# Optimization experiments

Hardware: AMD Instinct MI355X
Metric: run time of the kernel (lower is better)

## Reference

```python
import jax, jax.numpy as jnp
import numpy as np

H = 128   # hidden_size
NL = 3    # num_layers
R = 32    # water_rows (Water2sea_slice_num)
O = 48    # water_cols (Original_slice_len)
B = 64    # batch_size
F = 32    # input_size
L = R + O - 1  # Water2sea_slice_len (wavefront length)


def setup_inputs():
    key = jax.random.key(0)
    k1, k2, k3, k4 = jax.random.split(key, 4)
    stdv = 1.0 / np.sqrt(H)
    inp = jax.random.normal(k1, (B, R, O, F), dtype=jnp.float32)
    W_first = jax.random.uniform(k2, (6 * H, F + 2 * H), minval=-stdv, maxval=stdv, dtype=jnp.float32)
    W_other = jax.random.uniform(k3, (NL - 1, 6 * H, 4 * H), minval=-stdv, maxval=stdv, dtype=jnp.float32)
    Bias = jax.random.uniform(k4, (NL, 6 * H), minval=-stdv, maxval=stdv, dtype=jnp.float32)
    return {"input": inp, "W_first": W_first, "W_other": W_other, "Bias": Bias,
            "batch_size": B, "input_size": F, "flag": 0}


def _forward(inp, W_first, W_other, Bias, batch_size, input_size, flag):
    # permute: flag==0 -> [rows, batch, cols, feat]
    x = jnp.transpose(inp, (2, 0, 1, 3)) if flag == 1 else jnp.transpose(inp, (1, 0, 2, 3))
    Rn, bs, On, Fn = x.shape
    Ln = Rn + On - 1
    # wavefront-shifted input: row r occupies slices [r, r+On) (input_transfer)
    padded = jnp.pad(x, ((0, 0), (0, 0), (0, Rn - 1), (0, 0)))                 # [R,B,L,F]
    shifted = jax.vmap(lambda t, r: jnp.roll(t, r, axis=1))(padded, jnp.arange(Rn))
    a0 = shifted.reshape(Rn * bs, Ln, Fn)
    # bias applied to row-group g at slice s iff (s < Rn) and (g <= s)  [faithful to linear()]
    s_idx = jnp.arange(Ln)[:, None]
    g_idx = jnp.arange(Rn)[None, :]
    bias_mask = ((g_idx <= s_idx) & (s_idx < Rn)).astype(jnp.float32)          # [L,R]
    bias_mask = jnp.repeat(bias_mask, bs, axis=1)[..., None]                   # [L,RB,1]

    def run_layer(a, W, bvec):
        # a: [RB, L, feat]; W: [6H, feat+2H]; bvec: [6H]
        def step(carry, xs):
            h_row, h_col = carry
            a_s, m_s = xs
            z = jnp.concatenate([h_row, h_col, a_s], axis=-1)
            gate = z @ W.T + m_s * bvec                                        # [RB,6H]
            sig = jax.nn.sigmoid(gate[:, :4 * H])
            tnh = jnp.tanh(gate[:, 4 * H:])
            ur, orow, uc, ocol = jnp.split(sig, 4, axis=-1)
            ir, ic = jnp.split(tnh, 2, axis=-1)
            h_row_n = jnp.tanh((1.0 - ur) * h_row + ur * ir) * orow
            h_col_n = jnp.tanh((1.0 - uc) * h_col + uc * ic) * ocol
            out = jnp.concatenate([h_row_n, h_col_n], axis=-1)
            h_col_roll = jnp.roll(h_col_n, bs, axis=0)  # transfer col hidden to next row
            return (h_row_n, h_col_roll), (out, h_row_n, h_col_n)
        h0 = jnp.zeros((Rn * bs, H), a.dtype)
        _, (outs, hrows, hcols) = jax.lax.scan(step, (h0, h0), (jnp.swapaxes(a, 0, 1), bias_mask))
        return outs, hrows, hcols  # each [L, RB, *]

    row_saves, col_saves = [], []
    a = a0
    for layer in range(NL):
        W = W_first if layer == 0 else W_other[layer - 1]
        outs, hrows, hcols = run_layer(a, W, Bias[layer])
        hrows = hrows.reshape(Ln, Rn, bs, H)
        hcols = hcols.reshape(Ln, Rn, bs, H)
        # row r finishes at slice On-1+r; col hidden of last row-group saved for slices >= Rn-1
        row_saves.append(hrows[On - 1 + jnp.arange(Rn), jnp.arange(Rn)])       # [R,B,H]
        col_saves.append(hcols[Rn - 1:, Rn - 1])                               # [O,B,H]
        a = jnp.swapaxes(outs, 0, 1)                                           # [RB,L,2H]; dropout p=0 -> identity
    output_all_slice = a
    hidden_row_all = jnp.transpose(jnp.stack(row_saves), (2, 0, 1, 3))         # [B,NL,R,H]
    hidden_col_all = jnp.transpose(jnp.stack(col_saves), (2, 0, 1, 3))         # [B,NL,O,H]
    return output_all_slice, hidden_row_all, hidden_col_all


def reference(input, W_first, W_other, Bias, batch_size, input_size, flag):
    return _forward(input, W_first, W_other, Bias, batch_size, input_size, flag)
```

## Files before the change

### kernel.cpp

```cpp
#include <hip/hip_runtime.h>
#include <stdint.h>

#define HH   128
#define NLAY 3
#define RR   32
#define OO   48
#define BBX  64
#define FFX  32
#define LLX  (RR + OO - 1)
#define RBr  (RR * BBX)
#define N6   (6 * HH)
#define TSTEPS (LLX + NLAY - 1)
#define NBLOCKS 192

typedef unsigned short u16;
typedef __attribute__((ext_vector_type(8))) short short8;
typedef __attribute__((ext_vector_type(4))) float f32x4;

#define OFF_ABUF0 ((size_t)0)
#define SZ_ABUF0  ((size_t)LLX * RBr * FFX * 2)
#define OFF_HZ    (OFF_ABUF0 + SZ_ABUF0)
#define SZ_HZ     ((size_t)NLAY * 2 * RBr * 256 * 2)
#define OFF_BAR   (OFF_HZ + SZ_HZ)
#define SZ_BAR    ((size_t)4096)
#define SZ_STATE  (SZ_HZ + SZ_BAR)

__device__ __forceinline__ u16 f2b(float x) {
  uint32_t u = __float_as_uint(x);
  return (u16)((u + 0x7FFFu + ((u >> 16) & 1u)) >> 16);
}
__device__ __forceinline__ float rcp_(float x) { return __builtin_amdgcn_rcpf(x); }
__device__ __forceinline__ float sigmoidf_(float x) {
  return rcp_(1.0f + __expf(-x));
}
__device__ __forceinline__ float tanhf_(float x) {
  return 1.0f - 2.0f * rcp_(__expf(2.0f * x) + 1.0f);
}

__global__ __launch_bounds__(256) void k_prep_input(const float* __restrict__ inp,
                                                    u16* __restrict__ abuf0) {
  int idx = blockIdx.x * 256 + threadIdx.x;
  if (idx >= LLX * RBr * FFX) return;
  int f   = idx & (FFX - 1);
  int row = (idx >> 5) & (RBr - 1);
  int s   = idx / (RBr * FFX);
  int g = row >> 6, b = row & 63;
  int o = s - g;
  float v = (o >= 0 && o < OO) ? inp[((b * RR + g) * OO + o) * FFX + f] : 0.0f;
  abuf0[idx] = f2b(v);
}

__global__ __launch_bounds__(256) void k_zero(uint32_t* __restrict__ p, size_t nwords) {
  size_t i = (size_t)blockIdx.x * 256 + threadIdx.x;
  size_t stride = (size_t)gridDim.x * 256;
  for (; i < nwords; i += stride) p[i] = 0u;
}

__device__ __forceinline__ void step_barrier(uint32_t* barC, uint32_t target, bool light) {
  __syncthreads();
  if (threadIdx.x == 0) {
    if (!light) __threadfence();
    __hip_atomic_fetch_add(barC, 1u, __ATOMIC_RELAXED, __HIP_MEMORY_SCOPE_AGENT);
    while (__hip_atomic_load(barC, __ATOMIC_RELAXED, __HIP_MEMORY_SCOPE_AGENT) < target)
      __builtin_amdgcn_s_sleep(1);
    if (!light) __threadfence();
  }
  __syncthreads();
  if (light) asm volatile("buffer_inv" ::: "memory");
}

template <int KK>
__device__ __forceinline__ void stage_w(const float* __restrict__ Wsrc, int jblk,
                                        u16* __restrict__ Wl) {
  constexpr int NFRAG = (KK / 32) * 6;
  for (int e = threadIdx.x; e < NFRAG * 64; e += 512) {
    int kcm = e >> 6, ln = e & 63;
    int kc = kcm / 6, m = kcm - kc * 6;
    int fr2 = ln & 15, hi2 = ln >> 4;
    int srow = m * 128 + jblk * 16 + fr2;
    const float* src = Wsrc + (size_t)srow * KK + kc * 32 + hi2 * 8;
    short8 v;
#pragma unroll
    for (int x = 0; x < 8; ++x) v[x] = (short)f2b(src[x]);
    *(short8*)&Wl[(size_t)e * 8] = v;
  }
}

template <int KK>
__device__ __forceinline__ void persist_body(char* __restrict__ ws,
                                             const float* __restrict__ Bias_l,
                                             float* __restrict__ out,
                                             int layer, int jblk, int bblk, bool light,
                                             u16* __restrict__ Wl,
                                             float* __restrict__ hcl,
                                             uint32_t* __restrict__ barC) {
  constexpr int NCH = KK / 32;
  const int tid = threadIdx.x;
  const int lane = tid & 63, w = tid >> 6;
  const int fr = lane & 15, hi = lane >> 4;

  const int g0   = w * 4 + (fr >> 3);
  const int bcol = bblk * 8 + (fr & 7);
  const int arow[2] = { g0 * 64 + bcol, (g0 + 2) * 64 + bcol };
  const int arp[2]  = { ((g0 + 1) & 31) * 64 + bcol, ((g0 + 3) & 31) * 64 + bcol };
  const int j = jblk * 16 + fr;
  const u16* wfrag = &Wl[lane * 8];
  float bia[6];
#pragma unroll
  for (int m = 0; m < 6; ++m) bia[m] = Bias_l[m * 128 + j];

  u16*   hz_base  = (u16*)(ws + OFF_HZ) + (size_t)layer * 2 * RBr * 256;
  u16*   hzp_base = (u16*)(ws + OFF_HZ) + (size_t)(layer - 1) * 2 * RBr * 256;
  u16*   abuf0    = (u16*)(ws + OFF_ABUF0);
  float* hid_row  = out + (size_t)RBr * LLX * 256;
  float* hid_col  = hid_row + (size_t)BBX * NLAY * RR * HH;

  float hr_reg[2][4];
#pragma unroll
  for (int p = 0; p < 2; ++p)
#pragma unroll
    for (int q = 0; q < 4; ++q) hr_reg[p][q] = 0.0f;

  for (int t = 0; t < TSTEPS; ++t) {
    const int s = t - layer;
    if (s >= 0 && s < LLX) {
      const int sW = s & 1, sR = sW ^ 1;
      const u16* hzR = hz_base + (size_t)sR * RBr * 256;
      u16*       hzW = hz_base + (size_t)sW * RBr * 256;
      const u16* hzP = hzp_base + (size_t)sW * RBr * 256;
      const u16* ab_s = abuf0 + (size_t)s * RBr * FFX;
      const float* hcR = hcl + sR * 4352;
      float*       hcW = hcl + sW * 4352;

#pragma unroll
      for (int p = 0; p < 2; ++p) {
        if (w * 4 + 2 * p <= s) {
          auto LDK = [&](int kc) -> short8 {
            if (kc < 8)
              return *(const short8*)&hzR[arow[p] * 256 + kc * 32 + hi * 8];
            if constexpr (KK == 288) {
              return *(const short8*)&ab_s[arow[p] * FFX + hi * 8];
            } else {
              if (kc < 12)
                return *(const short8*)&hzP[arow[p] * 256 + (kc - 8) * 32 + hi * 8];
              return *(const short8*)&hzP[arp[p] * 256 + 128 + (kc - 12) * 32 + hi * 8];
            }
          };

          f32x4 z4 = {0.f, 0.f, 0.f, 0.f};
          f32x4 acc[6];
#pragma unroll
          for (int m = 0; m < 6; ++m) acc[m] = z4;

          short8 ring[3];
          ring[0] = LDK(0);
          ring[1] = LDK(1);
          ring[2] = LDK(2);
          __builtin_amdgcn_s_setprio(1);
#pragma unroll
          for (int kc = 0; kc < NCH; ++kc) {
            short8 a = ring[kc % 3];
            if (kc + 3 < NCH) ring[kc % 3] = LDK(kc + 3);
#pragma unroll
            for (int m = 0; m < 6; ++m) {
              short8 bv = *(const short8*)&wfrag[(size_t)(kc * 6 + m) * 512];
              acc[m] = __builtin_amdgcn_mfma_f32_16x16x32_bf16(a, bv, acc[m], 0, 0, 0);
            }
          }
          __builtin_amdgcn_s_setprio(0);

          const int g = w * 4 + 2 * p + (hi >> 1);
          const int gp = (g + 1) & (RR - 1);
          const float msk = (g <= s && s < RR) ? 1.0f : 0.0f;
          float mb[6];
#pragma unroll
          for (int m = 0; m < 6; ++m) mb[m] = msk * bia[m];
#pragma unroll
          for (int q = 0; q < 4; ++q) {
            const int lb = (hi & 1) * 4 + q;
            const int b  = bblk * 8 + lb;
            const int row = g * 64 + b;
            const int lrow = g * 8 + lb;
            const int rp = gp * 64 + b;
            const int lrp = gp * 8 + lb;
            float ur  = sigmoidf_(acc[0][q] + mb[0]);
            float orw = sigmoidf_(acc[1][q] + mb[1]);
            float uc  = sigmoidf_(acc[2][q] + mb[2]);
            float oc  = sigmoidf_(acc[3][q] + mb[3]);
            float ir  = tanhf_(acc[4][q] + mb[4]);
            float ic  = tanhf_(acc[5][q] + mb[5]);
            float hr_o = hr_reg[p][q];
            float hc_o = hcR[lrow * 17 + fr];
            float hr_n = tanhf_((1.0f - ur) * hr_o + ur * ir) * orw;
            float hc_n = tanhf_((1.0f - uc) * hc_o + uc * ic) * oc;
            hr_reg[p][q] = hr_n;
            hcW[lrp * 17 + fr] = hc_n;
            hzW[row * 256 + j] = f2b(hr_n);
            hzW[rp * 256 + HH + j] = f2b(hc_n);
            if (layer == 2) {
              out[((size_t)row * LLX + s) * 256 + j] = hr_n;
              out[((size_t)row * LLX + s) * 256 + HH + j] = hc_n;
            }
            if (s - g == OO - 1)
              hid_row[((size_t)(b * NLAY + layer) * RR + g) * HH + j] = hr_n;
            if (g == RR - 1 && s >= RR - 1)
              hid_col[((size_t)(b * NLAY + layer) * OO + (s - (RR - 1))) * HH + j] = hc_n;
          }
        } else {
          const int g = w * 4 + 2 * p + (hi >> 1);
          const int gp = (g + 1) & (RR - 1);
#pragma unroll
          for (int q = 0; q < 4; ++q) {
            const int lb = (hi & 1) * 4 + q;
            const int b  = bblk * 8 + lb;
            const int row = g * 64 + b;
            const int rp = gp * 64 + b;
            const int lrp = gp * 8 + lb;
            hcW[lrp * 17 + fr] = 0.0f;
            hzW[row * 256 + j] = 0;
            hzW[rp * 256 + HH + j] = 0;
            if (layer == 2) {
              out[((size_t)row * LLX + s) * 256 + j] = 0.0f;
              out[((size_t)row * LLX + s) * 256 + HH + j] = 0.0f;
            }
          }
        }
      }
    }
    step_barrier(barC, 24u * (uint32_t)(t + 1), light);
  }
}

__global__ __launch_bounds__(512) void k_persist(char* __restrict__ ws,
                                                 const float* __restrict__ Wf,
                                                 const float* __restrict__ Wo,
                                                 const float* __restrict__ Bias,
                                                 float* __restrict__ out) {
  __shared__ u16 Wl[49152];
  __shared__ float hcl[8704];
  __shared__ uint32_t sh_light;
  const int bx = blockIdx.x;
  const int layer = bx >> 6, jblk = (bx >> 3) & 7, bblk = bx & 7;
  const int tid = threadIdx.x;

  if (layer == 0) stage_w<288>(Wf, jblk, Wl);
  else            stage_w<512>(Wo + (size_t)(layer - 1) * N6 * 512, jblk, Wl);
  for (int e = tid; e < 8704; e += 512) hcl[e] = 0.0f;

  uint32_t xcc;
  asm volatile("s_getreg_b32 %0, hwreg(20, 0, 4)" : "=s"(xcc));
  uint32_t* barG  = (uint32_t*)(ws + OFF_BAR);
  uint32_t* barC  = (uint32_t*)(ws + OFF_BAR + 128 + (size_t)bblk * 128);
  uint32_t* table = (uint32_t*)(ws + OFF_BAR + 2048);
  __syncthreads();
  if (tid == 0) {
    __hip_atomic_store(&table[bx], xcc, __ATOMIC_RELAXED, __HIP_MEMORY_SCOPE_AGENT);
    __hip_atomic_fetch_add(barG, 1u, __ATOMIC_RELEASE, __HIP_MEMORY_SCOPE_AGENT);
    while (__hip_atomic_load(barG, __ATOMIC_ACQUIRE, __HIP_MEMORY_SCOPE_AGENT) < NBLOCKS)
      __builtin_amdgcn_s_sleep(1);
    uint32_t lt = 1u;
    for (int q2 = 0; q2 < 24; ++q2) {
      uint32_t v = __hip_atomic_load(&table[q2 * 8 + bblk], __ATOMIC_RELAXED,
                                     __HIP_MEMORY_SCOPE_AGENT);
      lt &= (v == xcc) ? 1u : 0u;
    }
    sh_light = lt;
  }
  __syncthreads();
  const bool light = (sh_light != 0u);

  const float* bias_l = Bias + layer * N6;
  if (layer == 0)
    persist_body<288>(ws, bias_l, out, 0, jblk, bblk, light, Wl, hcl, barC);
  else
    persist_body<512>(ws, bias_l, out, layer, jblk, bblk, light, Wl, hcl, barC);
}

extern "C" void kernel_launch(void* const* d_in, const int* in_sizes, int n_in,
                              void* d_out, int out_size, void* d_ws, size_t ws_size,
                              hipStream_t stream) {
  const float* inp  = (const float*)d_in[0];
  const float* Wf   = (const float*)d_in[1];
  const float* Wo   = (const float*)d_in[2];
  const float* Bias = (const float*)d_in[3];
  float* out = (float*)d_out;
  char* ws = (char*)d_ws;
  (void)in_sizes; (void)n_in; (void)out_size; (void)ws_size;

  k_prep_input<<<(LLX * RBr * FFX) / 256, 256, 0, stream>>>(inp, (u16*)(ws + OFF_ABUF0));
  k_zero<<<2048, 256, 0, stream>>>((uint32_t*)(ws + OFF_HZ), SZ_STATE / 4);
  k_persist<<<NBLOCKS, 512, 0, stream>>>(ws, Wf, Wo, Bias, out);
}
```

Measured before the change: 827.2 us.

## Replace atomic-counter barrier with per-slot flags plus leader epoch broadcast

The per-step group barrier changes from a single atomic fetch-add counter to per-block arrival slots that a leader block polls in parallel, and the leader then publishes an epoch word that the other blocks spin on. This is meant to remove contention from 24 blocks doing atomic adds on one word. The step body is also restructured so that all A-fragments for the second row pair are preloaded before the first epilogue runs, overlapping loads with the gate math, and launch bounds now request two blocks per CU. The exchange is higher register pressure and an extra hop through the leader on every step.

```diff
diff --git a/kernel.cpp b/kernel.cpp
--- a/kernel.cpp
+++ b/kernel.cpp
@@ -22,7 +22,7 @@
 #define OFF_HZ    (OFF_ABUF0 + SZ_ABUF0)
 #define SZ_HZ     ((size_t)NLAY * 2 * RBr * 256 * 2)
 #define OFF_BAR   (OFF_HZ + SZ_HZ)
-#define SZ_BAR    ((size_t)4096)
+#define SZ_BAR    ((size_t)32768)
 #define SZ_STATE  (SZ_HZ + SZ_BAR)
 
 __device__ __forceinline__ u16 f2b(float x) {
@@ -56,12 +56,28 @@
   for (; i < nwords; i += stride) p[i] = 0u;
 }
 
-__device__ __forceinline__ void step_barrier(uint32_t* barC, uint32_t target, bool light) {
+__device__ __forceinline__ void step_barrier(uint32_t* __restrict__ arrC,
+                                             uint32_t* __restrict__ epoC,
+                                             int myslot, bool leader,
+                                             uint32_t target, bool light, int tid) {
   __syncthreads();
-  if (threadIdx.x == 0) {
+  if (tid == 0) {
     if (!light) __threadfence();
-    __hip_atomic_fetch_add(barC, 1u, __ATOMIC_RELAXED, __HIP_MEMORY_SCOPE_AGENT);
-    while (__hip_atomic_load(barC, __ATOMIC_RELAXED, __HIP_MEMORY_SCOPE_AGENT) < target)
+    __hip_atomic_store(&arrC[myslot * 16], target, __ATOMIC_RELAXED,
+                       __HIP_MEMORY_SCOPE_AGENT);
+  }
+  if (leader) {
+    if (tid < 24) {
+      while (__hip_atomic_load(&arrC[tid * 16], __ATOMIC_RELAXED,
+                               __HIP_MEMORY_SCOPE_AGENT) < target)
+        __builtin_amdgcn_s_sleep(1);
+    }
+    __syncthreads();
+    if (tid == 0)
+      __hip_atomic_store(epoC, target, __ATOMIC_RELAXED, __HIP_MEMORY_SCOPE_AGENT);
+  }
+  if (tid == 0) {
+    while (__hip_atomic_load(epoC, __ATOMIC_RELAXED, __HIP_MEMORY_SCOPE_AGENT) < target)
       __builtin_amdgcn_s_sleep(1);
     if (!light) __threadfence();
   }
@@ -93,16 +109,21 @@
                                              int layer, int jblk, int bblk, bool light,
                                              u16* __restrict__ Wl,
                                              float* __restrict__ hcl,
-                                             uint32_t* __restrict__ barC) {
+                                             uint32_t* __restrict__ arrC,
+                                             uint32_t* __restrict__ epoC,
+                                             bool leader) {
   constexpr int NCH = KK / 32;
   const int tid = threadIdx.x;
   const int lane = tid & 63, w = tid >> 6;
   const int fr = lane & 15, hi = lane >> 4;
-
-  const int g0   = w * 4 + (fr >> 3);
-  const int bcol = bblk * 8 + (fr & 7);
-  const int arow[2] = { g0 * 64 + bcol, (g0 + 2) * 64 + bcol };
-  const int arp[2]  = { ((g0 + 1) & 31) * 64 + bcol, ((g0 + 3) & 31) * 64 + bcol };
+  const int myslot = layer * 8 + jblk;
+
+  const int g0    = w * 4 + (fr >> 3);
+  const int bcol  = bblk * 8 + (fr & 7);
+  const int arow0 = g0 * 64 + bcol;
+  const int arow1 = (g0 + 2) * 64 + bcol;
+  const int arp0  = ((g0 + 1) & 31) * 64 + bcol;
+  const int arp1  = ((g0 + 3) & 31) * 64 + bcol;
   const int j = jblk * 16 + fr;
   const u16* wfrag = &Wl[lane * 8];
   float bia[6];
@@ -132,110 +153,128 @@
       const float* hcR = hcl + sR * 4352;
       float*       hcW = hcl + sW * 4352;
 
-#pragma unroll
-      for (int p = 0; p < 2; ++p) {
-        if (w * 4 + 2 * p <= s) {
-          auto LDK = [&](int kc) -> short8 {
-            if (kc < 8)
-              return *(const short8*)&hzR[arow[p] * 256 + kc * 32 + hi * 8];
-            if constexpr (KK == 288) {
-              return *(const short8*)&ab_s[arow[p] * FFX + hi * 8];
-            } else {
-              if (kc < 12)
-                return *(const short8*)&hzP[arow[p] * 256 + (kc - 8) * 32 + hi * 8];
-              return *(const short8*)&hzP[arp[p] * 256 + 128 + (kc - 12) * 32 + hi * 8];
-            }
-          };
-
-          f32x4 z4 = {0.f, 0.f, 0.f, 0.f};
-          f32x4 acc[6];
-#pragma unroll
-          for (int m = 0; m < 6; ++m) acc[m] = z4;
-
-          short8 ring[3];
-          ring[0] = LDK(0);
-          ring[1] = LDK(1);
-          ring[2] = LDK(2);
-          __builtin_amdgcn_s_setprio(1);
-#pragma unroll
-          for (int kc = 0; kc < NCH; ++kc) {
-            short8 a = ring[kc % 3];
-            if (kc + 3 < NCH) ring[kc % 3] = LDK(kc + 3);
-#pragma unroll
-            for (int m = 0; m < 6; ++m) {
-              short8 bv = *(const short8*)&wfrag[(size_t)(kc * 6 + m) * 512];
-              acc[m] = __builtin_amdgcn_mfma_f32_16x16x32_bf16(a, bv, acc[m], 0, 0, 0);
-            }
+      const bool act0 = (w * 4 <= s);
+      const bool act1 = (w * 4 + 2 <= s);
+
+      auto LDK = [&](int ar, int arp2, int kc) -> short8 {
+        if (kc < 8)
+          return *(const short8*)&hzR[ar * 256 + kc * 32 + hi * 8];
+        if constexpr (KK == 288) {
+          return *(const short8*)&ab_s[ar * FFX + hi * 8];
+        } else {
+          if (kc < 12)
+            return *(const short8*)&hzP[ar * 256 + (kc - 8) * 32 + hi * 8];
+          return *(const short8*)&hzP[arp2 * 256 + 128 + (kc - 12) * 32 + hi * 8];
+        }
+      };
+
+      auto MFMA6 = [&](short8 (&pa)[NCH], f32x4 (&acc)[6]) {
+        __builtin_amdgcn_s_setprio(1);
+#pragma unroll
+        for (int kc = 0; kc < NCH; ++kc)
+#pragma unroll
+          for (int m = 0; m < 6; ++m) {
+            short8 bv = *(const short8*)&wfrag[(size_t)(kc * 6 + m) * 512];
+            acc[m] = __builtin_amdgcn_mfma_f32_16x16x32_bf16(pa[kc], bv, acc[m], 0, 0, 0);
           }
-          __builtin_amdgcn_s_setprio(0);
-
-          const int g = w * 4 + 2 * p + (hi >> 1);
-          const int gp = (g + 1) & (RR - 1);
-          const float msk = (g <= s && s < RR) ? 1.0f : 0.0f;
-          float mb[6];
-#pragma unroll
-          for (int m = 0; m < 6; ++m) mb[m] = msk * bia[m];
-#pragma unroll
-          for (int q = 0; q < 4; ++q) {
-            const int lb = (hi & 1) * 4 + q;
-            const int b  = bblk * 8 + lb;
-            const int row = g * 64 + b;
-            const int lrow = g * 8 + lb;
-            const int rp = gp * 64 + b;
-            const int lrp = gp * 8 + lb;
-            float ur  = sigmoidf_(acc[0][q] + mb[0]);
-            float orw = sigmoidf_(acc[1][q] + mb[1]);
-            float uc  = sigmoidf_(acc[2][q] + mb[2]);
-            float oc  = sigmoidf_(acc[3][q] + mb[3]);
-            float ir  = tanhf_(acc[4][q] + mb[4]);
-            float ic  = tanhf_(acc[5][q] + mb[5]);
-            float hr_o = hr_reg[p][q];
-            float hc_o = hcR[lrow * 17 + fr];
-            float hr_n = tanhf_((1.0f - ur) * hr_o + ur * ir) * orw;
-            float hc_n = tanhf_((1.0f - uc) * hc_o + uc * ic) * oc;
-            hr_reg[p][q] = hr_n;
-            hcW[lrp * 17 + fr] = hc_n;
-            hzW[row * 256 + j] = f2b(hr_n);
-            hzW[rp * 256 + HH + j] = f2b(hc_n);
-            if (layer == 2) {
-              out[((size_t)row * LLX + s) * 256 + j] = hr_n;
-              out[((size_t)row * LLX + s) * 256 + HH + j] = hc_n;
-            }
-            if (s - g == OO - 1)
-              hid_row[((size_t)(b * NLAY + layer) * RR + g) * HH + j] = hr_n;
-            if (g == RR - 1 && s >= RR - 1)
-              hid_col[((size_t)(b * NLAY + layer) * OO + (s - (RR - 1))) * HH + j] = hc_n;
+        __builtin_amdgcn_s_setprio(0);
+      };
+
+      auto EPI = [&](int p2, f32x4 (&A)[6], float (&hr)[4]) {
+        const int g = w * 4 + 2 * p2 + (hi >> 1);
+        const int gp = (g + 1) & (RR - 1);
+        const float msk = (g <= s && s < RR) ? 1.0f : 0.0f;
+        float mb[6];
+#pragma unroll
+        for (int m = 0; m < 6; ++m) mb[m] = msk * bia[m];
+#pragma unroll
+        for (int q = 0; q < 4; ++q) {
+          const int lb = (hi & 1) * 4 + q;
+          const int b  = bblk * 8 + lb;
+          const int row = g * 64 + b;
+          const int lrow = g * 8 + lb;
+          const int rp = gp * 64 + b;
+          const int lrp = gp * 8 + lb;
+          float ur  = sigmoidf_(A[0][q] + mb[0]);
+          float orw = sigmoidf_(A[1][q] + mb[1]);
+          float uc  = sigmoidf_(A[2][q] + mb[2]);
+          float oc  = sigmoidf_(A[3][q] + mb[3]);
+          float ir  = tanhf_(A[4][q] + mb[4]);
+          float ic  = tanhf_(A[5][q] + mb[5]);
+          float hr_o = hr[q];
+          float hc_o = hcR[lrow * 17 + fr];
+          float hr_n = tanhf_((1.0f - ur) * hr_o + ur * ir) * orw;
+          float hc_n = tanhf_((1.0f - uc) * hc_o + uc * ic) * oc;
+          hr[q] = hr_n;
+          hcW[lrp * 17 + fr] = hc_n;
+          hzW[row * 256 + j] = f2b(hr_n);
+          hzW[rp * 256 + HH + j] = f2b(hc_n);
+          if (layer == 2) {
+            out[((size_t)row * LLX + s) * 256 + j] = hr_n;
+            out[((size_t)row * LLX + s) * 256 + HH + j] = hc_n;
           }
-        } else {
-          const int g = w * 4 + 2 * p + (hi >> 1);
-          const int gp = (g + 1) & (RR - 1);
-#pragma unroll
-          for (int q = 0; q < 4; ++q) {
-            const int lb = (hi & 1) * 4 + q;
-            const int b  = bblk * 8 + lb;
-            const int row = g * 64 + b;
-            const int rp = gp * 64 + b;
-            const int lrp = gp * 8 + lb;
-            hcW[lrp * 17 + fr] = 0.0f;
-            hzW[row * 256 + j] = 0;
-            hzW[rp * 256 + HH + j] = 0;
-            if (layer == 2) {
-              out[((size_t)row * LLX + s) * 256 + j] = 0.0f;
-              out[((size_t)row * LLX + s) * 256 + HH + j] = 0.0f;
-            }
+          if (s - g == OO - 1)
+            hid_row[((size_t)(b * NLAY + layer) * RR + g) * HH + j] = hr_n;
+          if (g == RR - 1 && s >= RR - 1)
+            hid_col[((size_t)(b * NLAY + layer) * OO + (s - (RR - 1))) * HH + j] = hc_n;
+        }
+      };
+
+      auto ZST = [&](int p2) {
+        const int g = w * 4 + 2 * p2 + (hi >> 1);
+        const int gp = (g + 1) & (RR - 1);
+#pragma unroll
+        for (int q = 0; q < 4; ++q) {
+          const int lb = (hi & 1) * 4 + q;
+          const int b  = bblk * 8 + lb;
+          const int row = g * 64 + b;
+          const int rp = gp * 64 + b;
+          const int lrp = gp * 8 + lb;
+          hcW[lrp * 17 + fr] = 0.0f;
+          hzW[row * 256 + j] = 0;
+          hzW[rp * 256 + HH + j] = 0;
+          if (layer == 2) {
+            out[((size_t)row * LLX + s) * 256 + j] = 0.0f;
+            out[((size_t)row * LLX + s) * 256 + HH + j] = 0.0f;
           }
         }
+      };
+
+      f32x4 z4 = {0.f, 0.f, 0.f, 0.f};
+      f32x4 acc0[6];
+      if (act0) {
+        short8 pa0[NCH];
+#pragma unroll
+        for (int kc = 0; kc < NCH; ++kc) pa0[kc] = LDK(arow0, arp0, kc);
+#pragma unroll
+        for (int m = 0; m < 6; ++m) acc0[m] = z4;
+        MFMA6(pa0, acc0);
+      }
+      short8 pa1[NCH];
+      if (act1) {
+#pragma unroll
+        for (int kc = 0; kc < NCH; ++kc) pa1[kc] = LDK(arow1, arp1, kc);
+      }
+      if (act0) EPI(0, acc0, hr_reg[0]); else ZST(0);
+      if (act1) {
+        f32x4 acc1[6];
+#pragma unroll
+        for (int m = 0; m < 6; ++m) acc1[m] = z4;
+        MFMA6(pa1, acc1);
+        EPI(1, acc1, hr_reg[1]);
+      } else {
+        ZST(1);
       }
     }
-    step_barrier(barC, 24u * (uint32_t)(t + 1), light);
-  }
-}
-
-__global__ __launch_bounds__(512) void k_persist(char* __restrict__ ws,
-                                                 const float* __restrict__ Wf,
-                                                 const float* __restrict__ Wo,
-                                                 const float* __restrict__ Bias,
-                                                 float* __restrict__ out) {
+    step_barrier(arrC, epoC, myslot, leader, (uint32_t)(t + 1), light, tid);
+  }
+}
+
+__global__ __launch_bounds__(512, 2) void k_persist(char* __restrict__ ws,
+                                                    const float* __restrict__ Wf,
+                                                    const float* __restrict__ Wo,
+                                                    const float* __restrict__ Bias,
+                                                    float* __restrict__ out) {
   __shared__ u16 Wl[49152];
   __shared__ float hcl[8704];
   __shared__ uint32_t sh_light;
@@ -250,8 +289,10 @@
   uint32_t xcc;
   asm volatile("s_getreg_b32 %0, hwreg(20, 0, 4)" : "=s"(xcc));
   uint32_t* barG  = (uint32_t*)(ws + OFF_BAR);
-  uint32_t* barC  = (uint32_t*)(ws + OFF_BAR + 128 + (size_t)bblk * 128);
-  uint32_t* table = (uint32_t*)(ws + OFF_BAR + 2048);
+  uint32_t* table = (uint32_t*)(ws + OFF_BAR + 256);
+  uint32_t* arrC  = (uint32_t*)(ws + OFF_BAR + 4096 + (size_t)bblk * 2048);
+  uint32_t* epoC  = (uint32_t*)(ws + OFF_BAR + 24576 + (size_t)bblk * 256);
+  const bool leader = (layer == 0 && jblk == 0);
   __syncthreads();
   if (tid == 0) {
     __hip_atomic_store(&table[bx], xcc, __ATOMIC_RELAXED, __HIP_MEMORY_SCOPE_AGENT);
@@ -271,9 +312,11 @@
 
   const float* bias_l = Bias + layer * N6;
   if (layer == 0)
-    persist_body<288>(ws, bias_l, out, 0, jblk, bblk, light, Wl, hcl, barC);
+    persist_body<288>(ws, bias_l, out, 0, jblk, bblk, light, Wl, hcl,
+                      arrC, epoC, leader);
   else
-    persist_body<512>(ws, bias_l, out, layer, jblk, bblk, light, Wl, hcl, barC);
+    persist_body<512>(ws, bias_l, out, layer, jblk, bblk, light, Wl, hcl,
+                      arrC, epoC, leader);
 }
 
 extern "C" void kernel_launch(void* const* d_in, const int* in_sizes, int n_in,
```

After: 1.073 ms. 29.7% more time.

## Double threads per persistent block so each wave handles one row-group pair

Applied to the files above, without the earlier changes.

Raises the persistent kernel from 512 to 1024 threads per block, giving 16 waves that each own a single pair of row groups instead of two. Each wave now runs one 16-row MFMA tile per step rather than looping over two, so the per-step work is spread across more waves to shorten the serial critical path between barriers. The cost is doubled register pressure across the CU (launch_bounds 1024), a larger block-wide __syncthreads, and possible register spills.

```diff
diff --git a/kernel.cpp b/kernel.cpp
--- a/kernel.cpp
+++ b/kernel.cpp
@@ -73,7 +73,7 @@
 __device__ __forceinline__ void stage_w(const float* __restrict__ Wsrc, int jblk,
                                         u16* __restrict__ Wl) {
   constexpr int NFRAG = (KK / 32) * 6;
-  for (int e = threadIdx.x; e < NFRAG * 64; e += 512) {
+  for (int e = threadIdx.x; e < NFRAG * 64; e += 1024) {
     int kcm = e >> 6, ln = e & 63;
     int kc = kcm / 6, m = kcm - kc * 6;
     int fr2 = ln & 15, hi2 = ln >> 4;
@@ -99,10 +99,10 @@
   const int lane = tid & 63, w = tid >> 6;
   const int fr = lane & 15, hi = lane >> 4;
 
-  const int g0   = w * 4 + (fr >> 3);
+  const int g0   = w * 2 + (fr >> 3);
   const int bcol = bblk * 8 + (fr & 7);
-  const int arow[2] = { g0 * 64 + bcol, (g0 + 2) * 64 + bcol };
-  const int arp[2]  = { ((g0 + 1) & 31) * 64 + bcol, ((g0 + 3) & 31) * 64 + bcol };
+  const int arow = g0 * 64 + bcol;
+  const int arp  = ((g0 + 1) & 31) * 64 + bcol;
   const int j = jblk * 16 + fr;
   const u16* wfrag = &Wl[lane * 8];
   float bia[6];
@@ -115,11 +115,9 @@
   float* hid_row  = out + (size_t)RBr * LLX * 256;
   float* hid_col  = hid_row + (size_t)BBX * NLAY * RR * HH;
 
-  float hr_reg[2][4];
-#pragma unroll
-  for (int p = 0; p < 2; ++p)
-#pragma unroll
-    for (int q = 0; q < 4; ++q) hr_reg[p][q] = 0.0f;
+  float hr_reg[4];
+#pragma unroll
+  for (int q = 0; q < 4; ++q) hr_reg[q] = 0.0f;
 
   for (int t = 0; t < TSTEPS; ++t) {
     const int s = t - layer;
@@ -132,97 +130,94 @@
       const float* hcR = hcl + sR * 4352;
       float*       hcW = hcl + sW * 4352;
 
-#pragma unroll
-      for (int p = 0; p < 2; ++p) {
-        if (w * 4 + 2 * p <= s) {
-          auto LDK = [&](int kc) -> short8 {
-            if (kc < 8)
-              return *(const short8*)&hzR[arow[p] * 256 + kc * 32 + hi * 8];
-            if constexpr (KK == 288) {
-              return *(const short8*)&ab_s[arow[p] * FFX + hi * 8];
-            } else {
-              if (kc < 12)
-                return *(const short8*)&hzP[arow[p] * 256 + (kc - 8) * 32 + hi * 8];
-              return *(const short8*)&hzP[arp[p] * 256 + 128 + (kc - 12) * 32 + hi * 8];
-            }
-          };
-
-          f32x4 z4 = {0.f, 0.f, 0.f, 0.f};
-          f32x4 acc[6];
-#pragma unroll
-          for (int m = 0; m < 6; ++m) acc[m] = z4;
-
-          short8 ring[3];
-          ring[0] = LDK(0);
-          ring[1] = LDK(1);
-          ring[2] = LDK(2);
-          __builtin_amdgcn_s_setprio(1);
-#pragma unroll
-          for (int kc = 0; kc < NCH; ++kc) {
-            short8 a = ring[kc % 3];
-            if (kc + 3 < NCH) ring[kc % 3] = LDK(kc + 3);
-#pragma unroll
-            for (int m = 0; m < 6; ++m) {
-              short8 bv = *(const short8*)&wfrag[(size_t)(kc * 6 + m) * 512];
-              acc[m] = __builtin_amdgcn_mfma_f32_16x16x32_bf16(a, bv, acc[m], 0, 0, 0);
-            }
-          }
-          __builtin_amdgcn_s_setprio(0);
-
-          const int g = w * 4 + 2 * p + (hi >> 1);
-          const int gp = (g + 1) & (RR - 1);
-          const float msk = (g <= s && s < RR) ? 1.0f : 0.0f;
-          float mb[6];
-#pragma unroll
-          for (int m = 0; m < 6; ++m) mb[m] = msk * bia[m];
-#pragma unroll
-          for (int q = 0; q < 4; ++q) {
-            const int lb = (hi & 1) * 4 + q;
-            const int b  = bblk * 8 + lb;
-            const int row = g * 64 + b;
-            const int lrow = g * 8 + lb;
-            const int rp = gp * 64 + b;
-            const int lrp = gp * 8 + lb;
-            float ur  = sigmoidf_(acc[0][q] + mb[0]);
-            float orw = sigmoidf_(acc[1][q] + mb[1]);
-            float uc  = sigmoidf_(acc[2][q] + mb[2]);
-            float oc  = sigmoidf_(acc[3][q] + mb[3]);
-            float ir  = tanhf_(acc[4][q] + mb[4]);
-            float ic  = tanhf_(acc[5][q] + mb[5]);
-            float hr_o = hr_reg[p][q];
-            float hc_o = hcR[lrow * 17 + fr];
-            float hr_n = tanhf_((1.0f - ur) * hr_o + ur * ir) * orw;
-            float hc_n = tanhf_((1.0f - uc) * hc_o + uc * ic) * oc;
-            hr_reg[p][q] = hr_n;
-            hcW[lrp * 17 + fr] = hc_n;
-            hzW[row * 256 + j] = f2b(hr_n);
-            hzW[rp * 256 + HH + j] = f2b(hc_n);
-            if (layer == 2) {
-              out[((size_t)row * LLX + s) * 256 + j] = hr_n;
-              out[((size_t)row * LLX + s) * 256 + HH + j] = hc_n;
-            }
-            if (s - g == OO - 1)
-              hid_row[((size_t)(b * NLAY + layer) * RR + g) * HH + j] = hr_n;
-            if (g == RR - 1 && s >= RR - 1)
-              hid_col[((size_t)(b * NLAY + layer) * OO + (s - (RR - 1))) * HH + j] = hc_n;
-          }
-        } else {
-          const int g = w * 4 + 2 * p + (hi >> 1);
-          const int gp = (g + 1) & (RR - 1);
-#pragma unroll
-          for (int q = 0; q < 4; ++q) {
-            const int lb = (hi & 1) * 4 + q;
-            const int b  = bblk * 8 + lb;
-            const int row = g * 64 + b;
-            const int rp = gp * 64 + b;
-            const int lrp = gp * 8 + lb;
-            hcW[lrp * 17 + fr] = 0.0f;
-            hzW[row * 256 + j] = 0;
-            hzW[rp * 256 + HH + j] = 0;
-            if (layer == 2) {
-              out[((size_t)row * LLX + s) * 256 + j] = 0.0f;
-              out[((size_t)row * LLX + s) * 256 + HH + j] = 0.0f;
-            }
+      if (w * 2 <= s) {
+        auto LDK = [&](int kc) -> short8 {
+          if (kc < 8)
+            return *(const short8*)&hzR[arow * 256 + kc * 32 + hi * 8];
+          if constexpr (KK == 288) {
+            return *(const short8*)&ab_s[arow * FFX + hi * 8];
+          } else {
+            if (kc < 12)
+              return *(const short8*)&hzP[arow * 256 + (kc - 8) * 32 + hi * 8];
+            return *(const short8*)&hzP[arp * 256 + 128 + (kc - 12) * 32 + hi * 8];
+          }
+        };
+
+        f32x4 z4 = {0.f, 0.f, 0.f, 0.f};
+        f32x4 acc[6];
+#pragma unroll
+        for (int m = 0; m < 6; ++m) acc[m] = z4;
+
+        short8 ring[3];
+        ring[0] = LDK(0);
+        ring[1] = LDK(1);
+        ring[2] = LDK(2);
+        __builtin_amdgcn_s_setprio(1);
+#pragma unroll
+        for (int kc = 0; kc < NCH; ++kc) {
+          short8 a = ring[kc % 3];
+          if (kc + 3 < NCH) ring[kc % 3] = LDK(kc + 3);
+#pragma unroll
+          for (int m = 0; m < 6; ++m) {
+            short8 bv = *(const short8*)&wfrag[(size_t)(kc * 6 + m) * 512];
+            acc[m] = __builtin_amdgcn_mfma_f32_16x16x32_bf16(a, bv, acc[m], 0, 0, 0);
+          }
+        }
+        __builtin_amdgcn_s_setprio(0);
+
+        const int g = w * 2 + (hi >> 1);
+        const int gp = (g + 1) & (RR - 1);
+        const float msk = (g <= s && s < RR) ? 1.0f : 0.0f;
+        float mb[6];
+#pragma unroll
+        for (int m = 0; m < 6; ++m) mb[m] = msk * bia[m];
+#pragma unroll
+        for (int q = 0; q < 4; ++q) {
+          const int lb = (hi & 1) * 4 + q;
+          const int b  = bblk * 8 + lb;
+          const int row = g * 64 + b;
+          const int lrow = g * 8 + lb;
+          const int rp = gp * 64 + b;
+          const int lrp = gp * 8 + lb;
+          float ur  = sigmoidf_(acc[0][q] + mb[0]);
+          float orw = sigmoidf_(acc[1][q] + mb[1]);
+          float uc  = sigmoidf_(acc[2][q] + mb[2]);
+          float oc  = sigmoidf_(acc[3][q] + mb[3]);
+          float ir  = tanhf_(acc[4][q] + mb[4]);
+          float ic  = tanhf_(acc[5][q] + mb[5]);
+          float hr_o = hr_reg[q];
+          float hc_o = hcR[lrow * 17 + fr];
+          float hr_n = tanhf_((1.0f - ur) * hr_o + ur * ir) * orw;
+          float hc_n = tanhf_((1.0f - uc) * hc_o + uc * ic) * oc;
+          hr_reg[q] = hr_n;
+          hcW[lrp * 17 + fr] = hc_n;
+          hzW[row * 256 + j] = f2b(hr_n);
+          hzW[rp * 256 + HH + j] = f2b(hc_n);
+          if (layer == 2) {
+            out[((size_t)row * LLX + s) * 256 + j] = hr_n;
+            out[((size_t)row * LLX + s) * 256 + HH + j] = hc_n;
+          }
+          if (s - g == OO - 1)
+            hid_row[((size_t)(b * NLAY + layer) * RR + g) * HH + j] = hr_n;
+          if (g == RR - 1 && s >= RR - 1)
+            hid_col[((size_t)(b * NLAY + layer) * OO + (s - (RR - 1))) * HH + j] = hc_n;
+        }
+      } else {
+        const int g = w * 2 + (hi >> 1);
+        const int gp = (g + 1) & (RR - 1);
+#pragma unroll
+        for (int q = 0; q < 4; ++q) {
+          const int lb = (hi & 1) * 4 + q;
+          const int b  = bblk * 8 + lb;
+          const int row = g * 64 + b;
+          const int rp = gp * 64 + b;
+          const int lrp = gp * 8 + lb;
+          hcW[lrp * 17 + fr] = 0.0f;
+          hzW[row * 256 + j] = 0;
+          hzW[rp * 256 + HH + j] = 0;
+          if (layer == 2) {
+            out[((size_t)row * LLX + s) * 256 + j] = 0.0f;
+            out[((size_t)row * LLX + s) * 256 + HH + j] = 0.0f;
           }
         }
       }
@@ -231,11 +226,11 @@
   }
 }
 
-__global__ __launch_bounds__(512) void k_persist(char* __restrict__ ws,
-                                                 const float* __restrict__ Wf,
-                                                 const float* __restrict__ Wo,
-                                                 const float* __restrict__ Bias,
-                                                 float* __restrict__ out) {
+__global__ __launch_bounds__(1024, 4) void k_persist(char* __restrict__ ws,
+                                                     const float* __restrict__ Wf,
+                                                     const float* __restrict__ Wo,
+                                                     const float* __restrict__ Bias,
+                                                     float* __restrict__ out) {
   __shared__ u16 Wl[49152];
   __shared__ float hcl[8704];
   __shared__ uint32_t sh_light;
@@ -245,7 +240,7 @@
 
   if (layer == 0) stage_w<288>(Wf, jblk, Wl);
   else            stage_w<512>(Wo + (size_t)(layer - 1) * N6 * 512, jblk, Wl);
-  for (int e = tid; e < 8704; e += 512) hcl[e] = 0.0f;
+  for (int e = tid; e < 8704; e += 1024) hcl[e] = 0.0f;
 
   uint32_t xcc;
   asm volatile("s_getreg_b32 %0, hwreg(20, 0, 4)" : "=s"(xcc));
@@ -289,5 +284,5 @@
 
   k_prep_input<<<(LLX * RBr * FFX) / 256, 256, 0, stream>>>(inp, (u16*)(ws + OFF_ABUF0));
   k_zero<<<2048, 256, 0, stream>>>((uint32_t*)(ws + OFF_HZ), SZ_STATE / 4);
-  k_persist<<<NBLOCKS, 512, 0, stream>>>(ws, Wf, Wo, Bias, out);
-}
+  k_persist<<<NBLOCKS, 1024, 0, stream>>>(ws, Wf, Wo, Bias, out);
+}
```

Result: faster. 770.8 us (-6.8%).
